# Kernel tuning notes

Measured on AMD Instinct MI355X. Metric: run time of the kernel, lower is better.

The kernel has to match this reference:

```python
import jax, jax.numpy as jnp
import numpy as np

XYZ_MIN = jnp.array([-1.0, -1.0, -1.0], dtype=jnp.float32)
XYZ_MAX = jnp.array([1.0, 1.0, 1.0], dtype=jnp.float32)
ALPHA_INIT = 0.01
ACT_SHIFT = float(np.log(1.0 / (1.0 - ALPHA_INIT) - 1.0))
INTERVAL = 0.5  # stepsize * voxel_size_ratio
NEAR, FAR = 0.2, 1.8
N_RAYS, N_SAMPLES = 4096, 256
GRID = 160
K0_DIM = 12
VIEW_PE = 4
WIDTH = 128
DIM0 = 3 + 3 * VIEW_PE * 2 + K0_DIM  # 39


def trilinear(grid, pts):
    """grid: [X,Y,Z,C]; pts: [N,3] world coords -> [N,C] (align_corners=True, border clamp)."""
    sz = jnp.array(grid.shape[:3], dtype=pts.dtype)
    ijk = (pts - XYZ_MIN) / (XYZ_MAX - XYZ_MIN) * (sz - 1.0)
    ijk = jnp.clip(ijk, 0.0, sz - 1.0)
    lo = jnp.clip(jnp.floor(ijk).astype(jnp.int32), 0, jnp.array(grid.shape[:3], jnp.int32) - 2)
    f = ijk - lo.astype(pts.dtype)
    hi = lo + 1
    x0, y0, z0 = lo[:, 0], lo[:, 1], lo[:, 2]
    x1, y1, z1 = hi[:, 0], hi[:, 1], hi[:, 2]
    fx, fy, fz = f[:, 0:1], f[:, 1:2], f[:, 2:3]
    c00 = grid[x0, y0, z0] * (1 - fz) + grid[x0, y0, z1] * fz
    c01 = grid[x0, y1, z0] * (1 - fz) + grid[x0, y1, z1] * fz
    c10 = grid[x1, y0, z0] * (1 - fz) + grid[x1, y0, z1] * fz
    c11 = grid[x1, y1, z0] * (1 - fz) + grid[x1, y1, z1] * fz
    c0 = c00 * (1 - fy) + c01 * fy
    c1 = c10 * (1 - fy) + c11 * fy
    return c0 * (1 - fx) + c1 * fx


def setup_inputs() -> dict:
    key = jax.random.key(0)
    ks = jax.random.split(key, 8)
    rays_o = jax.random.uniform(ks[0], (N_RAYS, 3), jnp.float32, -0.3, 0.3)
    rays_d = jax.random.normal(ks[1], (N_RAYS, 3), jnp.float32)
    density = jax.random.normal(ks[2], (GRID, GRID, GRID), jnp.float32)
    k0 = jax.random.normal(ks[3], (K0_DIM, GRID, GRID, GRID), jnp.float32) * 0.1
    W0 = jax.random.normal(ks[4], (DIM0, WIDTH), jnp.float32) * (1.0 / np.sqrt(DIM0))
    b0 = jnp.zeros((WIDTH,), jnp.float32)
    W1 = jax.random.normal(ks[5], (WIDTH, WIDTH), jnp.float32) * (1.0 / np.sqrt(WIDTH))
    b1 = jnp.zeros((WIDTH,), jnp.float32)
    W2 = jax.random.normal(ks[6], (WIDTH, 3), jnp.float32) * (1.0 / np.sqrt(WIDTH))
    b2 = jnp.zeros((3,), jnp.float32)
    return {"rays_o": rays_o, "rays_d": rays_d, "density": density, "k0": k0,
            "W0": W0, "b0": b0, "W1": W1, "b1": b1, "W2": W2, "b2": b2}


def reference(rays_o, rays_d, density, k0, W0, b0, W1, b1, W2, b2):
    R, S = rays_o.shape[0], N_SAMPLES
    viewdirs = rays_d / jnp.linalg.norm(rays_d, axis=-1, keepdims=True)
    t = jnp.linspace(NEAR, FAR, S, dtype=rays_o.dtype)  # [S]
    pts = rays_o[:, None, :] + rays_d[:, None, :] * t[None, :, None]  # [R,S,3]
    ptsf = pts.reshape(-1, 3)

    # Raw2Alpha: alpha = 1 - (1 + exp(d + shift))^(-interval)
    sigma = trilinear(density[..., None], ptsf)[:, 0].reshape(R, S)
    alpha = 1.0 - jnp.power(1.0 + jnp.exp(sigma + ACT_SHIFT), -INTERVAL)

    # Alphas2Weights: per-ray exclusive cumprod of transmittance
    Tcum = jnp.cumprod(1.0 - alpha + 1e-10, axis=1)  # [R,S]
    T = jnp.concatenate([jnp.ones((R, 1), alpha.dtype), Tcum[:, :-1]], axis=1)
    weights = alpha * T
    alphainv_last = Tcum[:, -1]

    # k0 features + view positional encoding -> rgbnet MLP
    feat = trilinear(jnp.moveaxis(k0, 0, -1), ptsf).reshape(R, S, K0_DIM)
    freq = (2.0 ** jnp.arange(VIEW_PE)).astype(rays_o.dtype)  # [P]
    vf = viewdirs[:, :, None] * freq[None, None, :]  # [R,3,P]
    vemb = jnp.concatenate([viewdirs, jnp.sin(vf).reshape(R, -1), jnp.cos(vf).reshape(R, -1)], axis=-1)  # [R,27]
    x = jnp.concatenate([feat, jnp.broadcast_to(vemb[:, None, :], (R, S, vemb.shape[-1]))], axis=-1)  # [R,S,39]

    h = jax.nn.relu(x @ W0 + b0)
    h = jax.nn.relu(h @ W1 + b1)
    rgb = jax.nn.sigmoid(h @ W2 + b2)  # [R,S,3]

    # composite with white background
    rgb_marched = jnp.sum(weights[..., None] * rgb, axis=1) + alphainv_last[:, None]
    return rgb_marched
```

## Files before the change

### kernel.cpp

```cpp
#include <hip/hip_runtime.h>
#include <hip/hip_bf16.h>

#define NRAYS 4096
#define NS 256
#define G 160
#define G2 (160*160)
#define G3 (160*160*160)
#define K0DIM 12
#define WIDTH 128
#define CHUNK 32
#define NCHUNK 8
#define HBS 136
#define ACT_SHIFT_F (-4.5951198501345889f)
#define TNEAR 0.2f
#define TFAR 1.8f

typedef unsigned short u16;
typedef unsigned int u32;
typedef __attribute__((ext_vector_type(8))) short short8;
typedef __attribute__((ext_vector_type(4))) float floatx4;

#define W1F_IDX(kq, qs, n) (((((kq)<<2) + (qs)) * 128 + (n)) << 3)

__device__ __forceinline__ float bf2f(u16 u) {
    union { u32 i; float f; } v; v.i = ((u32)u) << 16; return v.f;
}
__device__ __forceinline__ u16 f2bf(float f) {
    union { float f; u32 u; } v; v.f = f;
    u32 r = v.u + 0x7FFFu + ((v.u >> 16) & 1u);
    return (u16)(r >> 16);
}

__device__ __forceinline__ float loadv(const float* p, int i) { return p[i]; }
__device__ __forceinline__ float loadv(const u16* p, int i)   { return bf2f(p[i]); }
__device__ __forceinline__ void storev(float* p, int i, float v) { p[i] = v; }
__device__ __forceinline__ void storev(u16* p, int i, float v)   { p[i] = f2bf(v); }

template <typename T> struct QT;
template <> struct QT<u16>   { using type = ushort4; };
template <> struct QT<float> { using type = float4;  };

__device__ __forceinline__ void zpair(const ushort4& q, int d, float& v0, float& v1) {
    u16 r0 = (d == 0) ? q.x : ((d == 1) ? q.y : q.z);
    u16 r1 = (d == 0) ? q.y : ((d == 1) ? q.z : q.w);
    v0 = bf2f(r0); v1 = bf2f(r1);
}
__device__ __forceinline__ void zpair(const float4& q, int d, float& v0, float& v1) {
    v0 = (d == 0) ? q.x : ((d == 1) ? q.y : q.z);
    v1 = (d == 0) ? q.y : ((d == 1) ? q.z : q.w);
}

struct CoordsE { int base; int d; float fx, fy, fz; };

__device__ __forceinline__ CoordsE coords_e(float px, float py, float pz) {
    float gx = fminf(fmaxf((px + 1.0f) * 79.5f, 0.0f), 159.0f);
    float gy = fminf(fmaxf((py + 1.0f) * 79.5f, 0.0f), 159.0f);
    float gz = fminf(fmaxf((pz + 1.0f) * 79.5f, 0.0f), 159.0f);
    int ix = (int)gx; if (ix > 158) ix = 158;
    int iy = (int)gy; if (iy > 158) iy = 158;
    int iz = (int)gz; if (iz > 158) iz = 158;
    int ze = iz & ~1; if (ze > 156) ze = 156;
    CoordsE c;
    c.base = (ix * G + iy) * G + ze;
    c.d = iz - ze;
    c.fx = gx - (float)ix; c.fy = gy - (float)iy; c.fz = gz - (float)iz;
    return c;
}

__global__ void decide_mode(const u16* __restrict__ rays_d_u16, int* __restrict__ mode) {
    if (blockIdx.x == 0 && threadIdx.x == 0) {
        int bad = 0;
        for (int i = 0; i < 128; i++) {
            u16 u = rays_d_u16[i];
            int e = (u >> 7) & 0xFF;
            int m = u & 0x7F;
            float v = bf2f(u);
            if (e == 0xFF || (e == 0 && m != 0) || fabsf(v) > 32.0f) bad++;
        }
        *mode = (bad >= 4) ? 1 : 0;
    }
}

template <typename T, typename OT, int MODE>
__global__ __launch_bounds__(256, 3)
void dvgo_fused(const T* __restrict__ rays_o, const T* __restrict__ rays_d,
                const T* __restrict__ density, const T* __restrict__ k0,
                const T* __restrict__ W0, const T* __restrict__ b0,
                const T* __restrict__ W1, const T* __restrict__ b1,
                const T* __restrict__ W2, const T* __restrict__ b2,
                OT* __restrict__ out, const int* __restrict__ mode)
{
    if (*mode != MODE) return;

    using qvec = typename QT<T>::type;

    __shared__ __align__(16) u16   W1f[WIDTH * WIDTH];
    __shared__ __align__(16) u16   h0B[CHUNK * HBS];
    __shared__ __align__(16) u16   W0f[WIDTH * 16];
    __shared__ __align__(16) u16   featB[CHUNK * 16];
    __shared__ __align__(16) float W2Tf[3 * WIDTH];
    __shared__ float p2[CHUNK * 6];
    __shared__ float base0[WIDTH];
    __shared__ float b1s[WIDTH];
    __shared__ float b2s[3];
    __shared__ float vembs[27];
    __shared__ float wts[NS];
    __shared__ float red[96];
    __shared__ float ainvs;

    const int r = blockIdx.x;
    const int tid = threadIdx.x;

    const float o0 = loadv(rays_o, r*3+0);
    const float o1 = loadv(rays_o, r*3+1);
    const float o2 = loadv(rays_o, r*3+2);
    const float d0 = loadv(rays_d, r*3+0);
    const float d1 = loadv(rays_d, r*3+1);
    const float d2 = loadv(rays_d, r*3+2);

    for (int idx = tid; idx < WIDTH*WIDTH; idx += 256) {
        int k = idx >> 7, n = idx & 127;
        W1f[W1F_IDX(k >> 5, (k >> 3) & 3, n) + (k & 7)] = f2bf(loadv(W1, idx));
    }
    for (int i = tid; i < WIDTH*16; i += 256) {
        int n = i >> 4, k = i & 15;
        W0f[i] = (k < K0DIM) ? f2bf(loadv(W0, k*WIDTH + n)) : (u16)0;
    }
    for (int i = tid; i < CHUNK*4; i += 256)
        featB[(i >> 2)*16 + 12 + (i & 3)] = 0;
    for (int k = tid; k < 3*WIDTH; k += 256) {
        int c = k >> 7, i = k & 127;
        W2Tf[k] = loadv(W2, i*3 + c);
    }
    if (tid < WIDTH) b1s[tid] = loadv(b1, tid);
    if (tid < 3)     b2s[tid] = loadv(b2, tid);

    if (tid < 27) {
        float inv = rsqrtf(d0*d0 + d1*d1 + d2*d2);
        float v0 = d0*inv, v1 = d1*inv, v2 = d2*inv;
        float val;
        if (tid < 3) {
            val = (tid == 0) ? v0 : ((tid == 1) ? v1 : v2);
        } else if (tid < 15) {
            int t2 = tid - 3; int dd = t2 >> 2; int p = t2 & 3;
            float vd = (dd == 0) ? v0 : ((dd == 1) ? v1 : v2);
            val = sinf(vd * (float)(1 << p));
        } else {
            int t2 = tid - 15; int dd = t2 >> 2; int p = t2 & 3;
            float vd = (dd == 0) ? v0 : ((dd == 1) ? v1 : v2);
            val = cosf(vd * (float)(1 << p));
        }
        vembs[tid] = val;
    }
    __syncthreads();

    if (tid < WIDTH) {
        float a = loadv(b0, tid);
        #pragma unroll
        for (int i = 0; i < 27; i++)
            a += vembs[i] * loadv(W0, (K0DIM + i)*WIDTH + tid);
        base0[tid] = a;
    }

    {
        int s = tid;
        float tv = TNEAR + (TFAR - TNEAR) * ((float)s * (1.0f/(float)(NS-1)));
        CoordsE c = coords_e(o0 + d0*tv, o1 + d1*tv, o2 + d2*tv);
        qvec q00 = *(const qvec*)(density + c.base);
        qvec q01 = *(const qvec*)(density + c.base + G);
        qvec q10 = *(const qvec*)(density + c.base + G2);
        qvec q11 = *(const qvec*)(density + c.base + G2 + G);
        float a0,a1,b0v,b1v,c0v,c1v,d0v,d1v;
        zpair(q00, c.d, a0, a1); zpair(q01, c.d, b0v, b1v);
        zpair(q10, c.d, c0v, c1v); zpair(q11, c.d, d0v, d1v);
        float c00 = a0*(1.0f-c.fz) + a1*c.fz;
        float c01 = b0v*(1.0f-c.fz) + b1v*c.fz;
        float c10 = c0v*(1.0f-c.fz) + c1v*c.fz;
        float c11 = d0v*(1.0f-c.fz) + d1v*c.fz;
        float e0 = c00*(1.0f-c.fy) + c01*c.fy;
        float e1 = c10*(1.0f-c.fy) + c11*c.fy;
        float sigma = e0*(1.0f-c.fx) + e1*c.fx;
        float alpha = 1.0f - rsqrtf(1.0f + __expf(sigma + ACT_SHIFT_F));
        wts[s] = alpha;
    }
    __syncthreads();

    if (tid == 0) {
        float w = 1.0f;
        for (int s = 0; s < NS; s++) {
            float a = wts[s];
            wts[s] = a * w;
            w *= (1.0f - a + 1e-10f);
        }
        ainvs = w;
    }
    __syncthreads();

    const int lane = tid & 63;
    const int wvid = tid >> 6;
    const int mt   = wvid & 1;
    const int nh   = wvid >> 1;
    const int q    = lane >> 4;
    const int ncol = lane & 15;
    const int arow = mt*16 + ncol;
    const int kcol = q * 8;
    const int drow0 = mt*16 + q*4;

    qvec qa[4], qb[4];
    CoordsE cea, ceb;
    const int ch0 = tid >> 5;
    const int sl0 = tid & 31;
    const int ch1 = 8 + (tid >> 5);
    const int sl1 = tid & 31;
    const bool has1 = (tid < 128);

    #define ISSUE_GATHER(CH, SL, C0N, Q, CE)                                    \
        { int s_ = (C0N) + (SL);                                                \
          float tv_ = TNEAR + (TFAR - TNEAR) * ((float)s_ * (1.0f/255.0f));     \
          CE = coords_e(o0 + d0*tv_, o1 + d1*tv_, o2 + d2*tv_);                 \
          const T* g_ = k0 + (size_t)(CH)*G3;                                   \
          Q[0] = *(const qvec*)(g_ + CE.base);                                  \
          Q[1] = *(const qvec*)(g_ + CE.base + G);                              \
          Q[2] = *(const qvec*)(g_ + CE.base + G2);                             \
          Q[3] = *(const qvec*)(g_ + CE.base + G2 + G); }

    #define COMMIT_GATHER(CH, SL, Q, CE)                                        \
        { float a0_,a1_,b0_,b1_,c0_,c1_,d0_,d1_;                                \
          zpair(Q[0], CE.d, a0_, a1_); zpair(Q[1], CE.d, b0_, b1_);             \
          zpair(Q[2], CE.d, c0_, c1_); zpair(Q[3], CE.d, d0_, d1_);             \
          float fz_ = CE.fz, fy_ = CE.fy, fx_ = CE.fx;                          \
          float c00_ = a0_*(1.0f-fz_) + a1_*fz_;                                \
          float c01_ = b0_*(1.0f-fz_) + b1_*fz_;                                \
          float c10_ = c0_*(1.0f-fz_) + c1_*fz_;                                \
          float c11_ = d0_*(1.0f-fz_) + d1_*fz_;                                \
          float e0_ = c00_*(1.0f-fy_) + c01_*fy_;                               \
          float e1_ = c10_*(1.0f-fy_) + c11_*fy_;                               \
          featB[(SL)*16 + (CH)] = f2bf(e0_*(1.0f-fx_) + e1_*fx_); }

    ISSUE_GATHER(ch0, sl0, 0, qa, cea);
    if (has1) ISSUE_GATHER(ch1, sl1, 0, qb, ceb);

    float rgbacc = 0.0f;

    for (int cc = 0; cc < NCHUNK; cc++) {
        const int c0 = cc * CHUNK;

        COMMIT_GATHER(ch0, sl0, qa, cea);
        if (has1) COMMIT_GATHER(ch1, sl1, qb, ceb);
        __syncthreads();

        {
            short8 af0 = {};
            short8 bf0 = {}, bf1 = {}, bf2v = {}, bf3 = {};
            if (q < 2) {
                af0  = *(const short8*)&featB[arow*16 + kcol];
                bf0  = *(const short8*)&W0f[(nh*64 +  0 + ncol)*16 + kcol];
                bf1  = *(const short8*)&W0f[(nh*64 + 16 + ncol)*16 + kcol];
                bf2v = *(const short8*)&W0f[(nh*64 + 32 + ncol)*16 + kcol];
                bf3  = *(const short8*)&W0f[(nh*64 + 48 + ncol)*16 + kcol];
            }
            floatx4 acc0[4];
            #pragma unroll
            for (int t = 0; t < 4; t++) {
                float v = base0[nh*64 + t*16 + ncol];
                acc0[t] = (floatx4){v, v, v, v};
            }
            acc0[0] = __builtin_amdgcn_mfma_f32_16x16x32_bf16(af0, bf0,  acc0[0], 0, 0, 0);
            acc0[1] = __builtin_amdgcn_mfma_f32_16x16x32_bf16(af0, bf1,  acc0[1], 0, 0, 0);
            acc0[2] = __builtin_amdgcn_mfma_f32_16x16x32_bf16(af0, bf2v, acc0[2], 0, 0, 0);
            acc0[3] = __builtin_amdgcn_mfma_f32_16x16x32_bf16(af0, bf3,  acc0[3], 0, 0, 0);
            #pragma unroll
            for (int t = 0; t < 4; t++) {
                int j = nh*64 + t*16 + ncol;
                #pragma unroll
                for (int rI = 0; rI < 4; rI++)
                    h0B[(drow0 + rI)*HBS + j] = f2bf(fmaxf(acc0[t][rI], 0.0f));
            }
        }
        __syncthreads();

        if (cc + 1 < NCHUNK) {
            ISSUE_GATHER(ch0, sl0, c0 + CHUNK, qa, cea);
            if (has1) ISSUE_GATHER(ch1, sl1, c0 + CHUNK, qb, ceb);
        }

        {
            floatx4 acc[4];
            #pragma unroll
            for (int t = 0; t < 4; t++) {
                float bj = b1s[nh*64 + t*16 + ncol];
                acc[t] = (floatx4){bj, bj, bj, bj};
            }
            #pragma unroll
            for (int kq = 0; kq < 4; kq++) {
                short8 af = *(const short8*)&h0B[arow*HBS + kq*32 + kcol];
                #pragma unroll
                for (int t = 0; t < 4; t++) {
                    short8 bf = *(const short8*)&W1f[W1F_IDX(kq, q, nh*64 + t*16 + ncol)];
                    acc[t] = __builtin_amdgcn_mfma_f32_16x16x32_bf16(af, bf, acc[t], 0, 0, 0);
                }
            }

            float p[3][4];
            #pragma unroll
            for (int c = 0; c < 3; c++)
                { p[c][0]=0; p[c][1]=0; p[c][2]=0; p[c][3]=0; }
            #pragma unroll
            for (int t = 0; t < 4; t++) {
                int j = nh*64 + t*16 + ncol;
                float w20 = W2Tf[j], w21 = W2Tf[WIDTH + j], w22 = W2Tf[2*WIDTH + j];
                #pragma unroll
                for (int rI = 0; rI < 4; rI++) {
                    float h = fmaxf(acc[t][rI], 0.0f);
                    p[0][rI] += h * w20;
                    p[1][rI] += h * w21;
                    p[2][rI] += h * w22;
                }
            }
            #pragma unroll
            for (int m = 1; m <= 8; m <<= 1) {
                #pragma unroll
                for (int c = 0; c < 3; c++) {
                    #pragma unroll
                    for (int rI = 0; rI < 4; rI++)
                        p[c][rI] += __shfl_xor(p[c][rI], m, 64);
                }
            }
            if (ncol == 0) {
                #pragma unroll
                for (int rI = 0; rI < 4; rI++) {
                    #pragma unroll
                    for (int c = 0; c < 3; c++)
                        p2[(drow0 + rI)*6 + nh*3 + c] = p[c][rI];
                }
            }
        }
        __syncthreads();

        if (tid < 96) {
            int c = tid >> 5, s = tid & 31;
            float acc2 = b2s[c] + p2[s*6 + c] + p2[s*6 + 3 + c];
            float rgb = 1.0f / (1.0f + __expf(-acc2));
            rgbacc += wts[c0 + s] * rgb;
        }
    }

    if (tid < 96) red[tid] = rgbacc;
    __syncthreads();
    if (tid < 3) {
        float s = 0.0f;
        #pragma unroll
        for (int k = 0; k < 32; k++) s += red[tid*32 + k];
        storev(out, r*3 + tid, s + ainvs);
    }
    #undef ISSUE_GATHER
    #undef COMMIT_GATHER
}

extern "C" void kernel_launch(void* const* d_in, const int* in_sizes, int n_in,
                              void* d_out, int out_size, void* d_ws, size_t ws_size,
                              hipStream_t stream) {
    int* mode = (int*)d_ws;
    decide_mode<<<dim3(1), dim3(64), 0, stream>>>((const u16*)d_in[1], mode);

    dvgo_fused<u16, u16, 0><<<dim3(NRAYS), dim3(256), 0, stream>>>(
        (const u16*)d_in[0], (const u16*)d_in[1], (const u16*)d_in[2],
        (const u16*)d_in[3], (const u16*)d_in[4], (const u16*)d_in[5],
        (const u16*)d_in[6], (const u16*)d_in[7], (const u16*)d_in[8],
        (const u16*)d_in[9], (u16*)d_out, mode);

    dvgo_fused<float, float, 1><<<dim3(NRAYS), dim3(256), 0, stream>>>(
        (const float*)d_in[0], (const float*)d_in[1], (const float*)d_in[2],
        (const float*)d_in[3], (const float*)d_in[4], (const float*)d_in[5],
        (const float*)d_in[6], (const float*)d_in[7], (const float*)d_in[8],
        (const float*)d_in[9], (float*)d_out, mode);
}
```

Baseline: 522.3 us.

## Transpose k0 grid to channel-last bf16 in workspace and gather interleaved

Adds a pre-pass kernel that converts k0 from channel-major to channel-last bf16 in the workspace, so each sample's 12 channels sit contiguously and the gathers hit fewer cache lines. The main kernel gains a layout-1 path that reads scalar bf16 corners from this buffer with a deeper two-chunk-ahead prefetch. The separate mode-decision kernel is dropped and each block votes on the dtype itself with __syncthreads_count. In exchange, every call pays for the full grid transpose (about 98 MB of bf16 written, more read in fp32), and the fast path depends on the workspace being large enough.

After: 611.5 us. 17.1% more time.

```diff
diff --git a/kernel.cpp b/kernel.cpp
--- a/kernel.cpp
+++ b/kernel.cpp
@@ -35,6 +35,8 @@
 __device__ __forceinline__ float loadv(const u16* p, int i)   { return bf2f(p[i]); }
 __device__ __forceinline__ void storev(float* p, int i, float v) { p[i] = v; }
 __device__ __forceinline__ void storev(u16* p, int i, float v)   { p[i] = f2bf(v); }
+__device__ __forceinline__ u16 as_bf16(u16 v)   { return v; }
+__device__ __forceinline__ u16 as_bf16(float v) { return f2bf(v); }
 
 template <typename T> struct QT;
 template <> struct QT<u16>   { using type = ushort4; };
@@ -50,8 +52,21 @@
     v1 = (d == 0) ? q.y : ((d == 1) ? q.z : q.w);
 }
 
+struct Coords { int idx; float fx, fy, fz; };
+__device__ __forceinline__ Coords coords_for(float px, float py, float pz) {
+    float gx = fminf(fmaxf((px + 1.0f) * 79.5f, 0.0f), 159.0f);
+    float gy = fminf(fmaxf((py + 1.0f) * 79.5f, 0.0f), 159.0f);
+    float gz = fminf(fmaxf((pz + 1.0f) * 79.5f, 0.0f), 159.0f);
+    int ix = (int)gx; if (ix > 158) ix = 158;
+    int iy = (int)gy; if (iy > 158) iy = 158;
+    int iz = (int)gz; if (iz > 158) iz = 158;
+    Coords c;
+    c.idx = (ix * G + iy) * G + iz;
+    c.fx = gx - (float)ix; c.fy = gy - (float)iy; c.fz = gz - (float)iz;
+    return c;
+}
+
 struct CoordsE { int base; int d; float fx, fy, fz; };
-
 __device__ __forceinline__ CoordsE coords_e(float px, float py, float pz) {
     float gx = fminf(fmaxf((px + 1.0f) * 79.5f, 0.0f), 159.0f);
     float gy = fminf(fmaxf((py + 1.0f) * 79.5f, 0.0f), 159.0f);
@@ -67,30 +82,57 @@
     return c;
 }
 
-__global__ void decide_mode(const u16* __restrict__ rays_d_u16, int* __restrict__ mode) {
-    if (blockIdx.x == 0 && threadIdx.x == 0) {
-        int bad = 0;
-        for (int i = 0; i < 128; i++) {
-            u16 u = rays_d_u16[i];
-            int e = (u >> 7) & 0xFF;
-            int m = u & 0x7F;
-            float v = bf2f(u);
-            if (e == 0xFF || (e == 0 && m != 0) || fabsf(v) > 32.0f) bad++;
-        }
-        *mode = (bad >= 4) ? 1 : 0;
-    }
-}
-
-template <typename T, typename OT, int MODE>
+__device__ __forceinline__ int wild16(u16 u) {
+    int e = (u >> 7) & 0xFF;
+    int m = u & 0x7F;
+    float v = bf2f(u);
+    return (e == 0xFF || (e == 0 && m != 0) || fabsf(v) > 32.0f) ? 1 : 0;
+}
+
+template <typename T, int MODE>
+__global__ __launch_bounds__(64)
+void transpose_k0(const T* __restrict__ k0, u16* __restrict__ outg,
+                  const u16* __restrict__ rdraw)
+{
+    const int tid = threadIdx.x;
+    int pred = wild16(rdraw[tid]) + wild16(rdraw[tid + 64]);
+    int bad = __syncthreads_count(pred != 0);
+    if ((bad >= 2) != (MODE == 1)) return;
+
+    const int b = blockIdx.x;
+    const int x = b / G, y = b - x * G;
+    const int colbase = (x * G + y) * G;
+
+    __shared__ __align__(4) u16 tile[G * 12];
+    #pragma unroll
+    for (int ch = 0; ch < 12; ch++)
+        for (int z = tid; z < G; z += 64)
+            tile[z * 12 + ch] = as_bf16(k0[(size_t)ch * G3 + colbase + z]);
+    __syncthreads();
+
+    const u32* t32 = (const u32*)tile;
+    u32* d32 = (u32*)outg;
+    const int obase = colbase * 6;
+    for (int i = tid; i < G * 6; i += 64) d32[obase + i] = t32[i];
+}
+
+template <typename T, typename OT, int MODE, int LAYOUT>
 __global__ __launch_bounds__(256, 3)
 void dvgo_fused(const T* __restrict__ rays_o, const T* __restrict__ rays_d,
                 const T* __restrict__ density, const T* __restrict__ k0,
                 const T* __restrict__ W0, const T* __restrict__ b0,
                 const T* __restrict__ W1, const T* __restrict__ b1,
                 const T* __restrict__ W2, const T* __restrict__ b2,
-                OT* __restrict__ out, const int* __restrict__ mode)
+                OT* __restrict__ out, const u16* __restrict__ rdraw,
+                const u16* __restrict__ wsgrid)
 {
-    if (*mode != MODE) return;
+    const int tid = threadIdx.x;
+
+    {
+        int pred = (tid < 128) ? wild16(rdraw[tid]) : 0;
+        int bad = __syncthreads_count(pred);
+        if ((bad >= 4) != (MODE == 1)) return;
+    }
 
     using qvec = typename QT<T>::type;
 
@@ -109,7 +151,6 @@
     __shared__ float ainvs;
 
     const int r = blockIdx.x;
-    const int tid = threadIdx.x;
 
     const float o0 = loadv(rays_o, r*3+0);
     const float o1 = loadv(rays_o, r*3+1);
@@ -206,143 +247,204 @@
     const int kcol = q * 8;
     const int drow0 = mt*16 + q*4;
 
-    qvec qa[4], qb[4];
-    CoordsE cea, ceb;
     const int ch0 = tid >> 5;
     const int sl0 = tid & 31;
     const int ch1 = 8 + (tid >> 5);
     const int sl1 = tid & 31;
     const bool has1 = (tid < 128);
 
-    #define ISSUE_GATHER(CH, SL, C0N, Q, CE)                                    \
-        { int s_ = (C0N) + (SL);                                                \
-          float tv_ = TNEAR + (TFAR - TNEAR) * ((float)s_ * (1.0f/255.0f));     \
-          CE = coords_e(o0 + d0*tv_, o1 + d1*tv_, o2 + d2*tv_);                 \
-          const T* g_ = k0 + (size_t)(CH)*G3;                                   \
-          Q[0] = *(const qvec*)(g_ + CE.base);                                  \
-          Q[1] = *(const qvec*)(g_ + CE.base + G);                              \
-          Q[2] = *(const qvec*)(g_ + CE.base + G2);                             \
-          Q[3] = *(const qvec*)(g_ + CE.base + G2 + G); }
-
-    #define COMMIT_GATHER(CH, SL, Q, CE)                                        \
-        { float a0_,a1_,b0_,b1_,c0_,c1_,d0_,d1_;                                \
-          zpair(Q[0], CE.d, a0_, a1_); zpair(Q[1], CE.d, b0_, b1_);             \
-          zpair(Q[2], CE.d, c0_, c1_); zpair(Q[3], CE.d, d0_, d1_);             \
-          float fz_ = CE.fz, fy_ = CE.fy, fx_ = CE.fx;                          \
-          float c00_ = a0_*(1.0f-fz_) + a1_*fz_;                                \
-          float c01_ = b0_*(1.0f-fz_) + b1_*fz_;                                \
-          float c10_ = c0_*(1.0f-fz_) + c1_*fz_;                                \
-          float c11_ = d0_*(1.0f-fz_) + d1_*fz_;                                \
-          float e0_ = c00_*(1.0f-fy_) + c01_*fy_;                               \
-          float e1_ = c10_*(1.0f-fy_) + c11_*fy_;                               \
-          featB[(SL)*16 + (CH)] = f2bf(e0_*(1.0f-fx_) + e1_*fx_); }
-
-    ISSUE_GATHER(ch0, sl0, 0, qa, cea);
-    if (has1) ISSUE_GATHER(ch1, sl1, 0, qb, ceb);
-
     float rgbacc = 0.0f;
 
-    for (int cc = 0; cc < NCHUNK; cc++) {
-        const int c0 = cc * CHUNK;
-
-        COMMIT_GATHER(ch0, sl0, qa, cea);
-        if (has1) COMMIT_GATHER(ch1, sl1, qb, ceb);
-        __syncthreads();
-
-        {
-            short8 af0 = {};
-            short8 bf0 = {}, bf1 = {}, bf2v = {}, bf3 = {};
-            if (q < 2) {
-                af0  = *(const short8*)&featB[arow*16 + kcol];
-                bf0  = *(const short8*)&W0f[(nh*64 +  0 + ncol)*16 + kcol];
-                bf1  = *(const short8*)&W0f[(nh*64 + 16 + ncol)*16 + kcol];
-                bf2v = *(const short8*)&W0f[(nh*64 + 32 + ncol)*16 + kcol];
-                bf3  = *(const short8*)&W0f[(nh*64 + 48 + ncol)*16 + kcol];
+    #define L0_BLOCK                                                            \
+        {                                                                       \
+            short8 af0 = {};                                                    \
+            short8 bf0 = {}, bf1 = {}, bf2v = {}, bf3 = {};                     \
+            if (q < 2) {                                                        \
+                af0  = *(const short8*)&featB[arow*16 + kcol];                  \
+                bf0  = *(const short8*)&W0f[(nh*64 +  0 + ncol)*16 + kcol];     \
+                bf1  = *(const short8*)&W0f[(nh*64 + 16 + ncol)*16 + kcol];     \
+                bf2v = *(const short8*)&W0f[(nh*64 + 32 + ncol)*16 + kcol];     \
+                bf3  = *(const short8*)&W0f[(nh*64 + 48 + ncol)*16 + kcol];     \
+            }                                                                   \
+            floatx4 acc0[4];                                                    \
+            _Pragma("unroll")                                                   \
+            for (int t = 0; t < 4; t++) {                                       \
+                float v = base0[nh*64 + t*16 + ncol];                           \
+                acc0[t] = (floatx4){v, v, v, v};                                \
+            }                                                                   \
+            acc0[0] = __builtin_amdgcn_mfma_f32_16x16x32_bf16(af0, bf0,  acc0[0], 0, 0, 0); \
+            acc0[1] = __builtin_amdgcn_mfma_f32_16x16x32_bf16(af0, bf1,  acc0[1], 0, 0, 0); \
+            acc0[2] = __builtin_amdgcn_mfma_f32_16x16x32_bf16(af0, bf2v, acc0[2], 0, 0, 0); \
+            acc0[3] = __builtin_amdgcn_mfma_f32_16x16x32_bf16(af0, bf3,  acc0[3], 0, 0, 0); \
+            _Pragma("unroll")                                                   \
+            for (int t = 0; t < 4; t++) {                                       \
+                int j = nh*64 + t*16 + ncol;                                    \
+                _Pragma("unroll")                                               \
+                for (int rI = 0; rI < 4; rI++)                                  \
+                    h0B[(drow0 + rI)*HBS + j] = f2bf(fmaxf(acc0[t][rI], 0.0f)); \
+            }                                                                   \
+        }
+
+    #define L1_L2_BLOCK(C0)                                                     \
+        {                                                                       \
+            floatx4 acc[4];                                                     \
+            _Pragma("unroll")                                                   \
+            for (int t = 0; t < 4; t++) {                                       \
+                float bj = b1s[nh*64 + t*16 + ncol];                            \
+                acc[t] = (floatx4){bj, bj, bj, bj};                             \
+            }                                                                   \
+            _Pragma("unroll")                                                   \
+            for (int kq = 0; kq < 4; kq++) {                                    \
+                short8 af = *(const short8*)&h0B[arow*HBS + kq*32 + kcol];      \
+                _Pragma("unroll")                                               \
+                for (int t = 0; t < 4; t++) {                                   \
+                    short8 bf = *(const short8*)&W1f[W1F_IDX(kq, q, nh*64 + t*16 + ncol)]; \
+                    acc[t] = __builtin_amdgcn_mfma_f32_16x16x32_bf16(af, bf, acc[t], 0, 0, 0); \
+                }                                                               \
+            }                                                                   \
+            float p[3][4];                                                      \
+            _Pragma("unroll")                                                   \
+            for (int c = 0; c < 3; c++)                                         \
+                { p[c][0]=0; p[c][1]=0; p[c][2]=0; p[c][3]=0; }                 \
+            _Pragma("unroll")                                                   \
+            for (int t = 0; t < 4; t++) {                                       \
+                int j = nh*64 + t*16 + ncol;                                    \
+                float w20 = W2Tf[j], w21 = W2Tf[WIDTH + j], w22 = W2Tf[2*WIDTH + j]; \
+                _Pragma("unroll")                                               \
+                for (int rI = 0; rI < 4; rI++) {                                \
+                    float h = fmaxf(acc[t][rI], 0.0f);                          \
+                    p[0][rI] += h * w20;                                        \
+                    p[1][rI] += h * w21;                                        \
+                    p[2][rI] += h * w22;                                        \
+                }                                                               \
+            }                                                                   \
+            _Pragma("unroll")                                                   \
+            for (int m = 1; m <= 8; m <<= 1) {                                  \
+                _Pragma("unroll")                                               \
+                for (int c = 0; c < 3; c++) {                                   \
+                    _Pragma("unroll")                                           \
+                    for (int rI = 0; rI < 4; rI++)                              \
+                        p[c][rI] += __shfl_xor(p[c][rI], m, 64);                \
+                }                                                               \
+            }                                                                   \
+            if (ncol == 0) {                                                    \
+                _Pragma("unroll")                                               \
+                for (int rI = 0; rI < 4; rI++) {                                \
+                    _Pragma("unroll")                                           \
+                    for (int c = 0; c < 3; c++)                                 \
+                        p2[(drow0 + rI)*6 + nh*3 + c] = p[c][rI];               \
+                }                                                               \
+            }                                                                   \
+        }
+
+    #define SIGMOID_ACC(C0)                                                     \
+        if (tid < 96) {                                                         \
+            int c = tid >> 5, s = tid & 31;                                     \
+            float acc2 = b2s[c] + p2[s*6 + c] + p2[s*6 + 3 + c];                \
+            float rgb = 1.0f / (1.0f + __expf(-acc2));                          \
+            rgbacc += wts[(C0) + s] * rgb;                                      \
+        }
+
+    if constexpr (LAYOUT == 1) {
+        #define ISSUE_I(CH, SL, C0N, RAW, FR)                                   \
+            { int s_ = (C0N) + (SL);                                            \
+              float tv_ = TNEAR + (TFAR - TNEAR) * ((float)s_ * (1.0f/255.0f)); \
+              Coords c_ = coords_for(o0 + d0*tv_, o1 + d1*tv_, o2 + d2*tv_);    \
+              int a_ = c_.idx*12 + (CH);                                        \
+              RAW[0] = wsgrid[a_];          RAW[1] = wsgrid[a_ + 12];           \
+              RAW[2] = wsgrid[a_ + 1920];   RAW[3] = wsgrid[a_ + 1932];         \
+              RAW[4] = wsgrid[a_ + 307200]; RAW[5] = wsgrid[a_ + 307212];       \
+              RAW[6] = wsgrid[a_ + 309120]; RAW[7] = wsgrid[a_ + 309132];       \
+              FR[0] = c_.fx; FR[1] = c_.fy; FR[2] = c_.fz; }
+
+        #define COMMIT_I(CH, SL, RAW, FR)                                       \
+            { float fz_ = FR[2], fy_ = FR[1], fx_ = FR[0];                      \
+              float c00_ = bf2f(RAW[0])*(1.0f-fz_) + bf2f(RAW[1])*fz_;          \
+              float c01_ = bf2f(RAW[2])*(1.0f-fz_) + bf2f(RAW[3])*fz_;          \
+              float c10_ = bf2f(RAW[4])*(1.0f-fz_) + bf2f(RAW[5])*fz_;          \
+              float c11_ = bf2f(RAW[6])*(1.0f-fz_) + bf2f(RAW[7])*fz_;          \
+              float e0_ = c00_*(1.0f-fy_) + c01_*fy_;                           \
+              float e1_ = c10_*(1.0f-fy_) + c11_*fy_;                           \
+              featB[(SL)*16 + (CH)] = f2bf(e0_*(1.0f-fx_) + e1_*fx_); }
+
+        #define CHUNK_BODY_I(C0, RA, FA, RB, FB)                                \
+            {                                                                   \
+                COMMIT_I(ch0, sl0, RA, FA);                                     \
+                if (has1) COMMIT_I(ch1, sl1, RB, FB);                           \
+                __syncthreads();                                                \
+                L0_BLOCK;                                                       \
+                __syncthreads();                                                \
+                if ((C0) + 64 < NS) {                                           \
+                    ISSUE_I(ch0, sl0, (C0) + 64, RA, FA);                       \
+                    if (has1) ISSUE_I(ch1, sl1, (C0) + 64, RB, FB);             \
+                }                                                               \
+                L1_L2_BLOCK(C0);                                                \
+                __syncthreads();                                                \
+                SIGMOID_ACC(C0);                                                \
             }
-            floatx4 acc0[4];
-            #pragma unroll
-            for (int t = 0; t < 4; t++) {
-                float v = base0[nh*64 + t*16 + ncol];
-                acc0[t] = (floatx4){v, v, v, v};
+
+        u16 rwA[8], rwB[8], rwC[8], rwD[8];
+        float fA[3], fB[3], fC[3], fD[3];
+        ISSUE_I(ch0, sl0, 0, rwA, fA);
+        if (has1) ISSUE_I(ch1, sl1, 0, rwB, fB);
+        ISSUE_I(ch0, sl0, 32, rwC, fC);
+        if (has1) ISSUE_I(ch1, sl1, 32, rwD, fD);
+
+        for (int cp = 0; cp < 4; cp++) {
+            int c0 = cp * 64;
+            CHUNK_BODY_I(c0,      rwA, fA, rwB, fB);
+            CHUNK_BODY_I(c0 + 32, rwC, fC, rwD, fD);
+        }
+        #undef ISSUE_I
+        #undef COMMIT_I
+        #undef CHUNK_BODY_I
+    } else {
+        qvec qa[4], qb[4];
+        CoordsE cea, ceb;
+
+        #define ISSUE_Q(CH, SL, C0N, Q, CE)                                     \
+            { int s_ = (C0N) + (SL);                                            \
+              float tv_ = TNEAR + (TFAR - TNEAR) * ((float)s_ * (1.0f/255.0f)); \
+              CE = coords_e(o0 + d0*tv_, o1 + d1*tv_, o2 + d2*tv_);             \
+              const T* g_ = k0 + (size_t)(CH)*G3;                               \
+              Q[0] = *(const qvec*)(g_ + CE.base);                              \
+              Q[1] = *(const qvec*)(g_ + CE.base + G);                          \
+              Q[2] = *(const qvec*)(g_ + CE.base + G2);                         \
+              Q[3] = *(const qvec*)(g_ + CE.base + G2 + G); }
+
+        #define COMMIT_Q(CH, SL, Q, CE)                                         \
+            { float a0_,a1_,b0_,b1_,c0_,c1_,d0_,d1_;                            \
+              zpair(Q[0], CE.d, a0_, a1_); zpair(Q[1], CE.d, b0_, b1_);         \
+              zpair(Q[2], CE.d, c0_, c1_); zpair(Q[3], CE.d, d0_, d1_);         \
+              float fz_ = CE.fz, fy_ = CE.fy, fx_ = CE.fx;                      \
+              float c00_ = a0_*(1.0f-fz_) + a1_*fz_;                            \
+              float c01_ = b0_*(1.0f-fz_) + b1_*fz_;                            \
+              float c10_ = c0_*(1.0f-fz_) + c1_*fz_;                            \
+              float c11_ = d0_*(1.0f-fz_) + d1_*fz_;                            \
+              float e0_ = c00_*(1.0f-fy_) + c01_*fy_;                           \
+              float e1_ = c10_*(1.0f-fy_) + c11_*fy_;                           \
+              featB[(SL)*16 + (CH)] = f2bf(e0_*(1.0f-fx_) + e1_*fx_); }
+
+        ISSUE_Q(ch0, sl0, 0, qa, cea);
+        if (has1) ISSUE_Q(ch1, sl1, 0, qb, ceb);
+
+        for (int cc = 0; cc < NCHUNK; cc++) {
+            const int c0 = cc * CHUNK;
+            COMMIT_Q(ch0, sl0, qa, cea);
+            if (has1) COMMIT_Q(ch1, sl1, qb, ceb);
+            __syncthreads();
+            L0_BLOCK;
+            __syncthreads();
+            if (cc + 1 < NCHUNK) {
+                ISSUE_Q(ch0, sl0, c0 + CHUNK, qa, cea);
+                if (has1) ISSUE_Q(ch1, sl1, c0 + CHUNK, qb, ceb);
             }
-            acc0[0] = __builtin_amdgcn_mfma_f32_16x16x32_bf16(af0, bf0,  acc0[0], 0, 0, 0);
-            acc0[1] = __builtin_amdgcn_mfma_f32_16x16x32_bf16(af0, bf1,  acc0[1], 0, 0, 0);
-            acc0[2] = __builtin_amdgcn_mfma_f32_16x16x32_bf16(af0, bf2v, acc0[2], 0, 0, 0);
-            acc0[3] = __builtin_amdgcn_mfma_f32_16x16x32_bf16(af0, bf3,  acc0[3], 0, 0, 0);
-            #pragma unroll
-            for (int t = 0; t < 4; t++) {
-                int j = nh*64 + t*16 + ncol;
-                #pragma unroll
-                for (int rI = 0; rI < 4; rI++)
-                    h0B[(drow0 + rI)*HBS + j] = f2bf(fmaxf(acc0[t][rI], 0.0f));
-            }
-        }
-        __syncthreads();
-
-        if (cc + 1 < NCHUNK) {
-            ISSUE_GATHER(ch0, sl0, c0 + CHUNK, qa, cea);
-            if (has1) ISSUE_GATHER(ch1, sl1, c0 + CHUNK, qb, ceb);
-        }
-
-        {
-            floatx4 acc[4];
-            #pragma unroll
-            for (int t = 0; t < 4; t++) {
-                float bj = b1s[nh*64 + t*16 + ncol];
-                acc[t] = (floatx4){bj, bj, bj, bj};
-            }
-            #pragma unroll
-            for (int kq = 0; kq < 4; kq++) {
-                short8 af = *(const short8*)&h0B[arow*HBS + kq*32 + kcol];
-                #pragma unroll
-                for (int t = 0; t < 4; t++) {
-                    short8 bf = *(const short8*)&W1f[W1F_IDX(kq, q, nh*64 + t*16 + ncol)];
-                    acc[t] = __builtin_amdgcn_mfma_f32_16x16x32_bf16(af, bf, acc[t], 0, 0, 0);
-                }
-            }
-
-            float p[3][4];
-            #pragma unroll
-            for (int c = 0; c < 3; c++)
-                { p[c][0]=0; p[c][1]=0; p[c][2]=0; p[c][3]=0; }
-            #pragma unroll
-            for (int t = 0; t < 4; t++) {
-                int j = nh*64 + t*16 + ncol;
-                float w20 = W2Tf[j], w21 = W2Tf[WIDTH + j], w22 = W2Tf[2*WIDTH + j];
-                #pragma unroll
-                for (int rI = 0; rI < 4; rI++) {
-                    float h = fmaxf(acc[t][rI], 0.0f);
-                    p[0][rI] += h * w20;
-                    p[1][rI] += h * w21;
-                    p[2][rI] += h * w22;
-                }
-            }
-            #pragma unroll
-            for (int m = 1; m <= 8; m <<= 1) {
-                #pragma unroll
-                for (int c = 0; c < 3; c++) {
-                    #pragma unroll
-                    for (int rI = 0; rI < 4; rI++)
-                        p[c][rI] += __shfl_xor(p[c][rI], m, 64);
-                }
-            }
-            if (ncol == 0) {
-                #pragma unroll
-                for (int rI = 0; rI < 4; rI++) {
-                    #pragma unroll
-                    for (int c = 0; c < 3; c++)
-                        p2[(drow0 + rI)*6 + nh*3 + c] = p[c][rI];
-                }
-            }
-        }
-        __syncthreads();
-
-        if (tid < 96) {
-            int c = tid >> 5, s = tid & 31;
-            float acc2 = b2s[c] + p2[s*6 + c] + p2[s*6 + 3 + c];
-            float rgb = 1.0f / (1.0f + __expf(-acc2));
-            rgbacc += wts[c0 + s] * rgb;
-        }
+            L1_L2_BLOCK(c0);
+            __syncthreads();
+            SIGMOID_ACC(c0);
+        }
+        #undef ISSUE_Q
+        #undef COMMIT_Q
     }
 
     if (tid < 96) red[tid] = rgbacc;
@@ -353,25 +455,45 @@
         for (int k = 0; k < 32; k++) s += red[tid*32 + k];
         storev(out, r*3 + tid, s + ainvs);
     }
-    #undef ISSUE_GATHER
-    #undef COMMIT_GATHER
+    #undef L0_BLOCK
+    #undef L1_L2_BLOCK
+    #undef SIGMOID_ACC
 }
 
 extern "C" void kernel_launch(void* const* d_in, const int* in_sizes, int n_in,
                               void* d_out, int out_size, void* d_ws, size_t ws_size,
                               hipStream_t stream) {
-    int* mode = (int*)d_ws;
-    decide_mode<<<dim3(1), dim3(64), 0, stream>>>((const u16*)d_in[1], mode);
-
-    dvgo_fused<u16, u16, 0><<<dim3(NRAYS), dim3(256), 0, stream>>>(
-        (const u16*)d_in[0], (const u16*)d_in[1], (const u16*)d_in[2],
-        (const u16*)d_in[3], (const u16*)d_in[4], (const u16*)d_in[5],
-        (const u16*)d_in[6], (const u16*)d_in[7], (const u16*)d_in[8],
-        (const u16*)d_in[9], (u16*)d_out, mode);
-
-    dvgo_fused<float, float, 1><<<dim3(NRAYS), dim3(256), 0, stream>>>(
-        (const float*)d_in[0], (const float*)d_in[1], (const float*)d_in[2],
-        (const float*)d_in[3], (const float*)d_in[4], (const float*)d_in[5],
-        (const float*)d_in[6], (const float*)d_in[7], (const float*)d_in[8],
-        (const float*)d_in[9], (float*)d_out, mode);
-}
+    const u16* rdraw = (const u16*)d_in[1];
+    const size_t grid_bytes = (size_t)G3 * 12 * 2;
+    const bool fast = (ws_size >= grid_bytes);
+
+    if (fast) {
+        u16* wsgrid = (u16*)d_ws;
+        transpose_k0<u16, 0><<<dim3(G*G), dim3(64), 0, stream>>>(
+            (const u16*)d_in[3], wsgrid, rdraw);
+        transpose_k0<float, 1><<<dim3(G*G), dim3(64), 0, stream>>>(
+            (const float*)d_in[3], wsgrid, rdraw);
+
+        dvgo_fused<u16, u16, 0, 1><<<dim3(NRAYS), dim3(256), 0, stream>>>(
+            (const u16*)d_in[0], (const u16*)d_in[1], (const u16*)d_in[2],
+            (const u16*)d_in[3], (const u16*)d_in[4], (const u16*)d_in[5],
+            (const u16*)d_in[6], (const u16*)d_in[7], (const u16*)d_in[8],
+            (const u16*)d_in[9], (u16*)d_out, rdraw, wsgrid);
+        dvgo_fused<float, float, 1, 1><<<dim3(NRAYS), dim3(256), 0, stream>>>(
+            (const float*)d_in[0], (const float*)d_in[1], (const float*)d_in[2],
+            (const float*)d_in[3], (const float*)d_in[4], (const float*)d_in[5],
+            (const float*)d_in[6], (const float*)d_in[7], (const float*)d_in[8],
+            (const float*)d_in[9], (float*)d_out, rdraw, wsgrid);
+    } else {
+        dvgo_fused<u16, u16, 0, 0><<<dim3(NRAYS), dim3(256), 0, stream>>>(
+            (const u16*)d_in[0], (const u16*)d_in[1], (const u16*)d_in[2],
+            (const u16*)d_in[3], (const u16*)d_in[4], (const u16*)d_in[5],
+            (const u16*)d_in[6], (const u16*)d_in[7], (const u16*)d_in[8],
+            (const u16*)d_in[9], (u16*)d_out, rdraw, nullptr);
+        dvgo_fused<float, float, 1, 0><<<dim3(NRAYS), dim3(256), 0, stream>>>(
+            (const float*)d_in[0], (const float*)d_in[1], (const float*)d_in[2],
+            (const float*)d_in[3], (const float*)d_in[4], (const float*)d_in[5],
+            (const float*)d_in[6], (const float*)d_in[7], (const float*)d_in[8],
+            (const float*)d_in[9], (float*)d_out, rdraw, nullptr);
+    }
+}
```
